# Performance work log

Hardware: AMD Instinct MI355X
Metric: run time of the kernel (lower is better)

Reference implementation:

```python
import jax, jax.numpy as jnp
import numpy as np

B, N, H2, FD, P = 8, 128, 800, 500, 100


def setup_inputs() -> dict:
    key = jax.random.key(0)
    ks = jax.random.split(key, 20)
    w = lambda k, shape, s=0.05: jax.random.normal(k, shape, dtype=jnp.float32) * s
    return {
        "hidden_out": jax.random.normal(ks[0], (B, N, H2), dtype=jnp.float32),
        "Wh": w(ks[1], (FD, H2)), "bh": w(ks[2], (FD,)),
        "Wm": w(ks[3], (FD, H2)), "bm": w(ks[4], (FD,)),
        "Ws": w(ks[5], (FD, H2)), "bs": w(ks[6], (FD,)),
        "Wg": w(ks[7], (FD, H2)), "bg": w(ks[8], (FD,)),
        "W_gp": w(ks[9], (P, 3 * FD)), "b_gp": w(ks[10], (P,)),
        "W_sp": w(ks[11], (P, 3 * FD)), "b_sp": w(ks[12], (P,)),
        "W_rp": w(ks[13], (P, 2 * FD)), "b_rp": w(ks[14], (P,)),
        "w_go": w(ks[15], (1, P)), "b_go": w(ks[16], (1,)),
        "w_so": w(ks[17], (1, P)), "b_so": w(ks[18], (1,)),
    }


def reference(hidden_out, Wh, bh, Wm, bm, Ws, bs, Wg, bg,
              W_gp, b_gp, W_sp, b_sp, W_rp, b_rp,
              w_go, b_go, w_so, b_so):
    # hidden_out: [B, n, 2H]. Scores indexed [b, i(modifier), k(grand/sib), j(head)].
    n = hidden_out.shape[1]
    Fd = Wh.shape[0]
    # tanh(cat(...)) is elementwise, so tanh each per-position projection.
    head = jnp.tanh(jnp.einsum('bnh,fh->bnf', hidden_out, Wh) + bh)
    mod  = jnp.tanh(jnp.einsum('bnh,fh->bnf', hidden_out, Wm) + bm)
    sib  = jnp.tanh(jnp.einsum('bnh,fh->bnf', hidden_out, Ws) + bs)
    grd  = jnp.tanh(jnp.einsum('bnh,fh->bnf', hidden_out, Wg) + bg)

    # grand_out(grand_preout(x)) is a composed linear map (no nonlinearity between),
    # so the score decomposes into per-position scalars.
    vg, vgh, vgm = [(w_go @ W_gp[:, a * Fd:(a + 1) * Fd]).ravel() for a in range(3)]
    c_g = (b_gp @ w_go.ravel()) + b_go[0]
    gk = grd @ vg   # [B, n] grand position k
    gj = head @ vgh  # [B, n] head position j
    gi = mod @ vgm   # [B, n] modifier position i
    grand_val = jnp.tanh(gi[:, :, None, None] + gk[:, None, :, None]
                         + gj[:, None, None, :] + c_g)  # [B, i, k, j]

    vsh, vss, vsm = [(w_so @ W_sp[:, a * Fd:(a + 1) * Fd]).ravel() for a in range(3)]
    c_s = (b_sp @ w_so.ravel()) + b_so[0]
    sk = head @ vsh  # s-head at position k
    sj = sib @ vss   # sibling at position j
    si = mod @ vsm   # s-modifier at position i
    sib_val = jnp.tanh(si[:, :, None, None] + sk[:, None, :, None]
                       + sj[:, None, None, :] + c_s)

    idx = jnp.arange(n)
    i_ = idx[:, None, None]
    k_ = idx[None, :, None]
    j_ = idx[None, None, :]
    valid = (i_ != 0) & (i_ != j_) & (j_ != k_)  # main triple-index branch

    grand_scores = jnp.where(valid, grand_val, -jnp.inf)
    sibling_scores = jnp.where(valid, sib_val, jnp.float32(0.0))

    # root branch: j = k = 0, i != 0; uses root_preout then grand_out.
    r0 = head[:, 0] @ (w_go @ W_rp[:, :Fd]).ravel()        # [B]
    ri = mod @ (w_go @ W_rp[:, Fd:]).ravel()                # [B, n]
    root = jnp.tanh(r0[:, None] + ri + (b_rp @ w_go.ravel()) + b_go[0])
    grand_scores = grand_scores.at[:, 1:, 0, 0].set(root[:, 1:])

    return grand_scores, sibling_scores
```

## Files before the change

### kernel.cpp

```cpp
#include <hip/hip_runtime.h>
#include <math.h>

#define FD 500
#define H2 800
#define NRR 1024
#define NPAD 2048
#define NKS 25

#define NEG_HUGE (-1.0e30f)

typedef __bf16 bf16x8 __attribute__((ext_vector_type(8)));
typedef float f32x4 __attribute__((ext_vector_type(4)));

union ChunkU { uint4 u; bf16x8 b; __bf16 h[8]; };

__device__ __forceinline__ float fast_tanh(float x) {
    float e = __expf(2.0f * x);
    return 1.0f - 2.0f / (e + 1.0f);
}

__device__ __forceinline__ bf16x8 as_frag(uint4 v) { ChunkU c; c.u = v; return c.b; }

__device__ __forceinline__ void gl_lds16(const uint4* g, uint4* lds) {
    __builtin_amdgcn_global_load_lds(
        (const __attribute__((address_space(1))) unsigned int*)g,
        (__attribute__((address_space(3))) unsigned int*)lds,
        16, 0, 0);
}

#define CV_STRIDE 164

__global__ __launch_bounds__(256) void convert_prep_kernel(
        const float* __restrict__ hidden,
        const float* __restrict__ Wh, const float* __restrict__ Wm,
        const float* __restrict__ Ws, const float* __restrict__ Wg,
        uint4* __restrict__ A_t, uint4* __restrict__ B_t,
        const float* __restrict__ W_gp, const float* __restrict__ b_gp,
        const float* __restrict__ W_sp, const float* __restrict__ b_sp,
        const float* __restrict__ W_rp, const float* __restrict__ b_rp,
        const float* __restrict__ w_go, const float* __restrict__ b_go,
        const float* __restrict__ w_so, const float* __restrict__ b_so,
        const float* __restrict__ bh, const float* __restrict__ bm,
        const float* __restrict__ bs, const float* __restrict__ bg,
        float* __restrict__ S8, float* __restrict__ bias_c,
        float* __restrict__ consts) {
    int blk = blockIdx.x;
    int t = threadIdx.x;

    if (blk == 272) {
        __shared__ float cr[3][128];
        if (t < 128) {
            cr[0][t] = (t < 100) ? b_gp[t] * w_go[t] : 0.f;
            cr[1][t] = (t < 100) ? b_sp[t] * w_so[t] : 0.f;
            cr[2][t] = (t < 100) ? b_rp[t] * w_go[t] : 0.f;
        }
        __syncthreads();
        for (int s = 64; s > 0; s >>= 1) {
            if (t < s) {
                cr[0][t] += cr[0][t+s];
                cr[1][t] += cr[1][t+s];
                cr[2][t] += cr[2][t+s];
            }
            __syncthreads();
        }
        if (t == 0) {
            consts[0] = cr[0][0] + b_go[0];
            consts[1] = cr[1][0] + b_so[0];
            consts[2] = cr[2][0] + b_go[0];
        }
        return;
    }

    if (blk >= 240) {
        __shared__ float racc[4][3][64];
        int pb = blk - 240;
        int j = t & 63;
        int e = t >> 6;
        int c = pb*64 + j;

        const float* v0 = nullptr; const float* v1 = nullptr; const float* v2 = nullptr;
        const float* m0 = nullptr; const float* m1 = nullptr; const float* m2 = nullptr;
        int o0 = 0, o1 = 0, o2 = 0, st0 = 0, st1 = 0, st2 = 0;
        int q0 = -1, q1 = -1, q2 = -1;
        float bias = 0.f;
        if (c < 2000) {
            int tt = c / FD, f = c % FD;
            if (tt == 0) {
                q0=1; v0=w_go; m0=W_gp; o0=500+f;  st0=1500;
                q1=5; v1=w_so; m1=W_sp; o1=f;      st1=1500;
                q2=7; v2=w_go; m2=W_rp; o2=f;      st2=1000;
                bias = bh[f];
            } else if (tt == 1) {
                q0=0; v0=w_go; m0=W_gp; o0=1000+f; st0=1500;
                q1=3; v1=w_so; m1=W_sp; o1=1000+f; st1=1500;
                q2=6; v2=w_go; m2=W_rp; o2=500+f;  st2=1000;
                bias = bm[f];
            } else if (tt == 2) {
                q0=4; v0=w_so; m0=W_sp; o0=500+f;  st0=1500;
                bias = bs[f];
            } else {
                q0=2; v0=w_go; m0=W_gp; o0=f;      st0=1500;
                bias = bg[f];
            }
        }
        float s0 = 0.f, s1 = 0.f, s2 = 0.f;
        int p0 = e * 25;
        #pragma unroll 5
        for (int p = p0; p < p0 + 25; ++p) {
            if (v0) s0 += v0[p] * m0[p*st0 + o0];
            if (v1) s1 += v1[p] * m1[p*st1 + o1];
            if (v2) s2 += v2[p] * m2[p*st2 + o2];
        }
        racc[e][0][j] = s0; racc[e][1][j] = s1; racc[e][2][j] = s2;
        __syncthreads();
        if (e == 0) {
            float v[8] = {0,0,0,0,0,0,0,0};
            float r0 = racc[0][0][j] + racc[1][0][j] + racc[2][0][j] + racc[3][0][j];
            float r1 = racc[0][1][j] + racc[1][1][j] + racc[2][1][j] + racc[3][1][j];
            float r2 = racc[0][2][j] + racc[1][2][j] + racc[2][2][j] + racc[3][2][j];
            if (q0 >= 0) v[q0] = r0;
            if (q1 >= 0) v[q1] = r1;
            if (q2 >= 0) v[q2] = r2;
            #pragma unroll
            for (int q = 0; q < 8; ++q) S8[q*NPAD + c] = v[q];
            bias_c[c] = bias;
        }
        return;
    }

    __shared__ float Ls[64 * CV_STRIDE];
    bool isA = blk < 80;
    int tile = isA ? (blk / 5) : ((blk - 80) / 5);
    int slab = isA ? (blk % 5) : ((blk - 80) % 5);

    #pragma unroll
    for (int i = 0; i < 10; ++i) {
        int idx = t + i*256;
        int row = idx / 40;
        int kq  = idx - row*40;
        float4 v = {0.f,0.f,0.f,0.f};
        if (isA) {
            int grow = tile*64 + row;
            v = *(const float4*)(hidden + (size_t)grow*H2 + slab*160 + kq*4);
        } else {
            int c = tile*64 + row;
            if (c < 2000) {
                int wt = c / FD, wf = c % FD;
                const float* wm = (wt==0)?Wh:(wt==1)?Wm:(wt==2)?Ws:Wg;
                v = *(const float4*)(wm + (size_t)wf*H2 + slab*160 + kq*4);
            }
        }
        *(float4*)&Ls[row*CV_STRIDE + kq*4] = v;
    }
    __syncthreads();

    int f = t >> 6, l = t & 63;
    int lrow  = f*16 + (l & 15);
    int koff0 = (l >> 4) * 8;
    uint4* dstbase = (isA ? A_t : B_t) + (size_t)tile * NKS * 512;
    #pragma unroll
    for (int ksl = 0; ksl < 5; ++ksl) {
        int ks = slab*5 + ksl;
        const float* src = &Ls[lrow*CV_STRIDE + ksl*32 + koff0];
        ChunkU hc, lo;
        #pragma unroll
        for (int j = 0; j < 8; ++j) {
            float x = src[j];
            __bf16 h = (__bf16)x;
            hc.h[j] = h;
            lo.h[j] = (__bf16)(x - (float)h);
        }
        uint4* dst = dstbase + (size_t)ks * 512;
        dst[(0*4 + f)*64 + l] = hc.u;
        dst[(1*4 + f)*64 + l] = lo.u;
    }
}

__global__ __launch_bounds__(256, 2) void gemm_kernel(
        const uint4* __restrict__ A_t, const uint4* __restrict__ B_t,
        const float* __restrict__ S8, const float* __restrict__ bias_c,
        float* __restrict__ partials) {
    __shared__ uint4 Abuf[4][512];
    __shared__ uint4 Bbuf[4][512];
    int tid = threadIdx.x;

    int lin = blockIdx.y * 32 + blockIdx.x;
    int xcd = lin & 7;
    int w   = lin >> 3;
    int rb  = (xcd & 1)*8 + (w & 7);
    int cb  = (xcd >> 1)*8 + (w >> 3);

    int l  = tid & 63;
    int wid = tid >> 6;
    int wr = wid >> 1, wc = wid & 1;
    int fa = wr*2, fb = wc*2;

    bool stA = wid < 2;
    int half = wid & 1;
    const uint4* sblk = (stA ? A_t + (size_t)rb * NKS * 512
                             : B_t + (size_t)cb * NKS * 512) + half*256;

    #define STAGE(buf, ks) do { \
        const uint4* sg_ = sblk + (ks)*512 + l; \
        uint4* db_ = (stA ? &Abuf[buf][0] : &Bbuf[buf][0]) + half*256; \
        gl_lds16(sg_,       db_); \
        gl_lds16(sg_ + 64,  db_ + 64); \
        gl_lds16(sg_ + 128, db_ + 128); \
        gl_lds16(sg_ + 192, db_ + 192); } while(0)

    f32x4 acc00 = {0.f,0.f,0.f,0.f}, acc01 = {0.f,0.f,0.f,0.f};
    f32x4 acc10 = {0.f,0.f,0.f,0.f}, acc11 = {0.f,0.f,0.f,0.f};

    #define COMPUTE(cur) do { \
        const uint4* Ab_ = &Abuf[cur][0]; \
        const uint4* Bb_ = &Bbuf[cur][0]; \
        bf16x8 ah0 = as_frag(Ab_[(fa+0)*64+l]), ah1 = as_frag(Ab_[(fa+1)*64+l]); \
        bf16x8 al0 = as_frag(Ab_[(4+fa+0)*64+l]), al1 = as_frag(Ab_[(4+fa+1)*64+l]); \
        bf16x8 bh0 = as_frag(Bb_[(fb+0)*64+l]), bh1 = as_frag(Bb_[(fb+1)*64+l]); \
        bf16x8 bl0 = as_frag(Bb_[(4+fb+0)*64+l]), bl1 = as_frag(Bb_[(4+fb+1)*64+l]); \
        acc00 = __builtin_amdgcn_mfma_f32_16x16x32_bf16(ah0, bh0, acc00,0,0,0); \
        acc00 = __builtin_amdgcn_mfma_f32_16x16x32_bf16(ah0, bl0, acc00,0,0,0); \
        acc00 = __builtin_amdgcn_mfma_f32_16x16x32_bf16(al0, bh0, acc00,0,0,0); \
        acc01 = __builtin_amdgcn_mfma_f32_16x16x32_bf16(ah0, bh1, acc01,0,0,0); \
        acc01 = __builtin_amdgcn_mfma_f32_16x16x32_bf16(ah0, bl1, acc01,0,0,0); \
        acc01 = __builtin_amdgcn_mfma_f32_16x16x32_bf16(al0, bh1, acc01,0,0,0); \
        acc10 = __builtin_amdgcn_mfma_f32_16x16x32_bf16(ah1, bh0, acc10,0,0,0); \
        acc10 = __builtin_amdgcn_mfma_f32_16x16x32_bf16(ah1, bl0, acc10,0,0,0); \
        acc10 = __builtin_amdgcn_mfma_f32_16x16x32_bf16(al1, bh0, acc10,0,0,0); \
        acc11 = __builtin_amdgcn_mfma_f32_16x16x32_bf16(ah1, bh1, acc11,0,0,0); \
        acc11 = __builtin_amdgcn_mfma_f32_16x16x32_bf16(ah1, bl1, acc11,0,0,0); \
        acc11 = __builtin_amdgcn_mfma_f32_16x16x32_bf16(al1, bh1, acc11,0,0,0); } while(0)

    STAGE(0, 0);
    STAGE(1, 1);

    for (int ks = 0; ks < NKS; ++ks) {
        if (ks + 2 < NKS) STAGE((ks + 2) & 3, ks + 2);
        if (ks < NKS - 2) {
            asm volatile("s_waitcnt vmcnt(4)" ::: "memory");
        } else {
            asm volatile("s_waitcnt vmcnt(0)" ::: "memory");
        }
        __builtin_amdgcn_s_barrier();
        __builtin_amdgcn_sched_barrier(0);
        COMPUTE(ks & 3);
    }
    asm volatile("s_waitcnt vmcnt(0) lgkmcnt(0)" ::: "memory");
    __builtin_amdgcn_s_barrier();
    #undef STAGE
    #undef COMPUTE

    int lr = l >> 4, lc = l & 15;
    float* Y = (float*)Abuf;
    {
        int col0 = (wc*2 + 0)*16 + lc;
        int col1 = (wc*2 + 1)*16 + lc;
        float bias0 = bias_c[cb*64 + col0], bias1 = bias_c[cb*64 + col1];
        int rb0 = (wr*2 + 0)*16 + lr*4;
        int rb1 = (wr*2 + 1)*16 + lr*4;
        #pragma unroll
        for (int r=0;r<4;++r) {
            Y[(rb0 + r)*64 + col0] = fast_tanh(acc00[r] + bias0);
            Y[(rb0 + r)*64 + col1] = fast_tanh(acc01[r] + bias1);
            Y[(rb1 + r)*64 + col0] = fast_tanh(acc10[r] + bias0);
            Y[(rb1 + r)*64 + col1] = fast_tanh(acc11[r] + bias1);
        }
    }
    __syncthreads();
    #pragma unroll
    for (int it=0; it<2; ++it) {
        int task = tid + it*256;
        int q = task & 7, row = task >> 3;
        const float4* s8r = (const float4*)(S8 + q*NPAD + cb*64);
        const float4* yr  = (const float4*)(Y + row*64);
        float s = 0.f;
        #pragma unroll
        for (int c4=0;c4<16;++c4) {
            float4 a = yr[c4], b = s8r[c4];
            s += a.x*b.x + a.y*b.y + a.z*b.z + a.w*b.w;
        }
        partials[((size_t)cb*NRR + rb*64 + row)*8 + q] = s;
    }
}

__global__ __launch_bounds__(256) void fill2_kernel(
        const float* __restrict__ partials, const float* __restrict__ consts,
        float* __restrict__ grand, float* __restrict__ sib) {
    int bi = blockIdx.x;
    int b = bi >> 7;
    int i = bi & 127;
    int tid = threadIdx.x;

    __shared__ float ph[256][4];
    __shared__ float gks[128], sks[128], Egj[128], Esj[128];
    __shared__ float own[4];

    {
        int r = tid & 127, half = tid >> 7;
        int grow = b*128 + r;
        float gj=0.f, gk=0.f, sj=0.f, sk=0.f;
        #pragma unroll 4
        for (int cc = 0; cc < 16; ++cc) {
            const float* p = partials + (size_t)(half*16 + cc)*8192 + (size_t)grow*8;
            gj += p[1]; gk += p[2]; sj += p[4]; sk += p[5];
        }
        ph[tid][0]=gj; ph[tid][1]=gk; ph[tid][2]=sj; ph[tid][3]=sk;
    }
    __syncthreads();
    if (tid < 128) {
        float gj = ph[tid][0] + ph[tid+128][0];
        float gk = ph[tid][1] + ph[tid+128][1];
        float sj = ph[tid][2] + ph[tid+128][2];
        float sk = ph[tid][3] + ph[tid+128][3];
        gks[tid] = gk; sks[tid] = sk;
        Egj[tid] = __expf(2.f * gj);
        Esj[tid] = __expf(2.f * sj);
    } else if (tid < 132) {
        int t2 = tid - 128;
        int grow = (t2 == 3) ? b*128 : (b*128 + i);
        int q = (t2==0) ? 0 : (t2==1) ? 3 : (t2==2) ? 6 : 7;
        float s = 0.f;
        #pragma unroll 8
        for (int cbk = 0; cbk < 32; ++cbk)
            s += partials[(size_t)cbk*8192 + (size_t)grow*8 + q];
        own[t2] = s;
    }
    __syncthreads();

    float gic = own[0] + consts[0];
    float sic = own[1] + consts[1];
    float rootv = fast_tanh(own[3] + own[2] + consts[2]);

    size_t base = (size_t)bi * (128*128);
    int j4 = (tid & 31) * 4;
    int klo = tid >> 5;

    for (int it = 0; it < 16; ++it) {
        int k = it*8 + klo;
        float Eg = __expf(2.f * (gic + gks[k]));
        float Es = __expf(2.f * (sic + sks[k]));
        float4 go, so;
        #pragma unroll
        for (int jj = 0; jj < 4; ++jj) {
            int j = j4 + jj;
            bool valid = (i != 0) && (i != j) && (j != k);
            float tg = Eg * Egj[j];
            float ts = Es * Esj[j];
            float g = 1.f - 2.f * __builtin_amdgcn_rcpf(tg + 1.f);
            float s = 1.f - 2.f * __builtin_amdgcn_rcpf(ts + 1.f);
            g = valid ? g : NEG_HUGE;
            s = valid ? s : 0.0f;
            if (i != 0 && k == 0 && j == 0) g = rootv;
            (&go.x)[jj] = g;
            (&so.x)[jj] = s;
        }
        size_t off = base + (size_t)k*128 + j4;
        *(float4*)(grand + off) = go;
        *(float4*)(sib + off) = so;
    }
}

extern "C" void kernel_launch(void* const* d_in, const int* in_sizes, int n_in,
                              void* d_out, int out_size, void* d_ws, size_t ws_size,
                              hipStream_t stream) {
    const float* hidden = (const float*)d_in[0];
    const float* Wh  = (const float*)d_in[1];   const float* bh  = (const float*)d_in[2];
    const float* Wm  = (const float*)d_in[3];   const float* bm  = (const float*)d_in[4];
    const float* Ws_ = (const float*)d_in[5];   const float* bs  = (const float*)d_in[6];
    const float* Wg  = (const float*)d_in[7];   const float* bg  = (const float*)d_in[8];
    const float* W_gp = (const float*)d_in[9];  const float* b_gp = (const float*)d_in[10];
    const float* W_sp = (const float*)d_in[11]; const float* b_sp = (const float*)d_in[12];
    const float* W_rp = (const float*)d_in[13]; const float* b_rp = (const float*)d_in[14];
    const float* w_go = (const float*)d_in[15]; const float* b_go = (const float*)d_in[16];
    const float* w_so = (const float*)d_in[17]; const float* b_so = (const float*)d_in[18];

    float* out   = (float*)d_out;
    float* grand = out;
    float* sib   = out + (size_t)16777216;

    uint4* A_t = (uint4*)out;
    uint4* B_t = (uint4*)out + 204800;

    float* S8      = (float*)d_ws;
    float* bias_c  = S8 + 16384;
    float* consts  = bias_c + 2048;
    float* partials= consts + 16;

    convert_prep_kernel<<<dim3(273), dim3(256), 0, stream>>>(
        hidden, Wh, Wm, Ws_, Wg, A_t, B_t,
        W_gp, b_gp, W_sp, b_sp, W_rp, b_rp, w_go, b_go, w_so, b_so,
        bh, bm, bs, bg, S8, bias_c, consts);
    gemm_kernel<<<dim3(32,16), dim3(256), 0, stream>>>(A_t, B_t, S8, bias_c, partials);
    fill2_kernel<<<dim3(1024), dim3(256), 0, stream>>>(partials, consts, grand, sib);
}
```

Measured before the change: 84.61 us.

## Fuse fp32-to-bf16 hi/lo split into GEMM, loading fp32 directly to LDS

Removes the separate conversion pass that wrote pre-split bf16 hi/lo tiles of hidden and the weights to scratch. The GEMM now streams raw fp32 rows straight into LDS with global_load_lds and splits them into hi/lo bf16 fragments in registers before each MFMA group. This drops one kernel's full read and write of the operands, and the prep kernel shrinks to only the small vector reductions. In exchange the GEMM redoes the conversion once per tile that reuses each operand, and its global loads become strided row reads instead of pre-packed contiguous chunks.

New measurement: 94.26 us. 11.4% more time.

```diff
diff --git a/kernel.cpp b/kernel.cpp
--- a/kernel.cpp
+++ b/kernel.cpp
@@ -19,22 +19,31 @@
     return 1.0f - 2.0f / (e + 1.0f);
 }
 
-__device__ __forceinline__ bf16x8 as_frag(uint4 v) { ChunkU c; c.u = v; return c.b; }
-
-__device__ __forceinline__ void gl_lds16(const uint4* g, uint4* lds) {
+__device__ __forceinline__ void gl_lds16(const float* g, uint4* lds) {
     __builtin_amdgcn_global_load_lds(
         (const __attribute__((address_space(1))) unsigned int*)g,
         (__attribute__((address_space(3))) unsigned int*)lds,
         16, 0, 0);
 }
 
-#define CV_STRIDE 164
-
-__global__ __launch_bounds__(256) void convert_prep_kernel(
-        const float* __restrict__ hidden,
-        const float* __restrict__ Wh, const float* __restrict__ Wm,
-        const float* __restrict__ Ws, const float* __restrict__ Wg,
-        uint4* __restrict__ A_t, uint4* __restrict__ B_t,
+__device__ __forceinline__ void cvt_hilo(uint4 x0, uint4 x1, bf16x8& hi, bf16x8& lo) {
+    union { uint4 u; float f[4]; } a, b;
+    a.u = x0; b.u = x1;
+    ChunkU h, m;
+    #pragma unroll
+    for (int j = 0; j < 4; ++j) {
+        float x = a.f[j]; __bf16 hh = (__bf16)x;
+        h.h[j] = hh; m.h[j] = (__bf16)(x - (float)hh);
+    }
+    #pragma unroll
+    for (int j = 0; j < 4; ++j) {
+        float x = b.f[j]; __bf16 hh = (__bf16)x;
+        h.h[4+j] = hh; m.h[4+j] = (__bf16)(x - (float)hh);
+    }
+    hi = h.b; lo = m.b;
+}
+
+__global__ __launch_bounds__(256) void prep_kernel(
         const float* __restrict__ W_gp, const float* __restrict__ b_gp,
         const float* __restrict__ W_sp, const float* __restrict__ b_sp,
         const float* __restrict__ W_rp, const float* __restrict__ b_rp,
@@ -47,7 +56,7 @@
     int blk = blockIdx.x;
     int t = threadIdx.x;
 
-    if (blk == 272) {
+    if (blk == 32) {
         __shared__ float cr[3][128];
         if (t < 128) {
             cr[0][t] = (t < 100) ? b_gp[t] * w_go[t] : 0.f;
@@ -71,113 +80,64 @@
         return;
     }
 
-    if (blk >= 240) {
-        __shared__ float racc[4][3][64];
-        int pb = blk - 240;
-        int j = t & 63;
-        int e = t >> 6;
-        int c = pb*64 + j;
-
-        const float* v0 = nullptr; const float* v1 = nullptr; const float* v2 = nullptr;
-        const float* m0 = nullptr; const float* m1 = nullptr; const float* m2 = nullptr;
-        int o0 = 0, o1 = 0, o2 = 0, st0 = 0, st1 = 0, st2 = 0;
-        int q0 = -1, q1 = -1, q2 = -1;
-        float bias = 0.f;
-        if (c < 2000) {
-            int tt = c / FD, f = c % FD;
-            if (tt == 0) {
-                q0=1; v0=w_go; m0=W_gp; o0=500+f;  st0=1500;
-                q1=5; v1=w_so; m1=W_sp; o1=f;      st1=1500;
-                q2=7; v2=w_go; m2=W_rp; o2=f;      st2=1000;
-                bias = bh[f];
-            } else if (tt == 1) {
-                q0=0; v0=w_go; m0=W_gp; o0=1000+f; st0=1500;
-                q1=3; v1=w_so; m1=W_sp; o1=1000+f; st1=1500;
-                q2=6; v2=w_go; m2=W_rp; o2=500+f;  st2=1000;
-                bias = bm[f];
-            } else if (tt == 2) {
-                q0=4; v0=w_so; m0=W_sp; o0=500+f;  st0=1500;
-                bias = bs[f];
-            } else {
-                q0=2; v0=w_go; m0=W_gp; o0=f;      st0=1500;
-                bias = bg[f];
-            }
-        }
-        float s0 = 0.f, s1 = 0.f, s2 = 0.f;
-        int p0 = e * 25;
-        #pragma unroll 5
-        for (int p = p0; p < p0 + 25; ++p) {
-            if (v0) s0 += v0[p] * m0[p*st0 + o0];
-            if (v1) s1 += v1[p] * m1[p*st1 + o1];
-            if (v2) s2 += v2[p] * m2[p*st2 + o2];
-        }
-        racc[e][0][j] = s0; racc[e][1][j] = s1; racc[e][2][j] = s2;
-        __syncthreads();
-        if (e == 0) {
-            float v[8] = {0,0,0,0,0,0,0,0};
-            float r0 = racc[0][0][j] + racc[1][0][j] + racc[2][0][j] + racc[3][0][j];
-            float r1 = racc[0][1][j] + racc[1][1][j] + racc[2][1][j] + racc[3][1][j];
-            float r2 = racc[0][2][j] + racc[1][2][j] + racc[2][2][j] + racc[3][2][j];
-            if (q0 >= 0) v[q0] = r0;
-            if (q1 >= 0) v[q1] = r1;
-            if (q2 >= 0) v[q2] = r2;
-            #pragma unroll
-            for (int q = 0; q < 8; ++q) S8[q*NPAD + c] = v[q];
-            bias_c[c] = bias;
-        }
-        return;
-    }
-
-    __shared__ float Ls[64 * CV_STRIDE];
-    bool isA = blk < 80;
-    int tile = isA ? (blk / 5) : ((blk - 80) / 5);
-    int slab = isA ? (blk % 5) : ((blk - 80) % 5);
-
-    #pragma unroll
-    for (int i = 0; i < 10; ++i) {
-        int idx = t + i*256;
-        int row = idx / 40;
-        int kq  = idx - row*40;
-        float4 v = {0.f,0.f,0.f,0.f};
-        if (isA) {
-            int grow = tile*64 + row;
-            v = *(const float4*)(hidden + (size_t)grow*H2 + slab*160 + kq*4);
+    __shared__ float racc[4][3][64];
+    int j = t & 63;
+    int e = t >> 6;
+    int c = blk*64 + j;
+
+    const float* v0 = nullptr; const float* v1 = nullptr; const float* v2 = nullptr;
+    const float* m0 = nullptr; const float* m1 = nullptr; const float* m2 = nullptr;
+    int o0 = 0, o1 = 0, o2 = 0, st0 = 0, st1 = 0, st2 = 0;
+    int q0 = -1, q1 = -1, q2 = -1;
+    float bias = 0.f;
+    if (c < 2000) {
+        int tt = c / FD, f = c % FD;
+        if (tt == 0) {
+            q0=1; v0=w_go; m0=W_gp; o0=500+f;  st0=1500;
+            q1=5; v1=w_so; m1=W_sp; o1=f;      st1=1500;
+            q2=7; v2=w_go; m2=W_rp; o2=f;      st2=1000;
+            bias = bh[f];
+        } else if (tt == 1) {
+            q0=0; v0=w_go; m0=W_gp; o0=1000+f; st0=1500;
+            q1=3; v1=w_so; m1=W_sp; o1=1000+f; st1=1500;
+            q2=6; v2=w_go; m2=W_rp; o2=500+f;  st2=1000;
+            bias = bm[f];
+        } else if (tt == 2) {
+            q0=4; v0=w_so; m0=W_sp; o0=500+f;  st0=1500;
+            bias = bs[f];
         } else {
-            int c = tile*64 + row;
-            if (c < 2000) {
-                int wt = c / FD, wf = c % FD;
-                const float* wm = (wt==0)?Wh:(wt==1)?Wm:(wt==2)?Ws:Wg;
-                v = *(const float4*)(wm + (size_t)wf*H2 + slab*160 + kq*4);
-            }
-        }
-        *(float4*)&Ls[row*CV_STRIDE + kq*4] = v;
-    }
+            q0=2; v0=w_go; m0=W_gp; o0=f;      st0=1500;
+            bias = bg[f];
+        }
+    }
+    float s0 = 0.f, s1 = 0.f, s2 = 0.f;
+    int p0 = e * 25;
+    #pragma unroll 5
+    for (int p = p0; p < p0 + 25; ++p) {
+        if (v0) s0 += v0[p] * m0[p*st0 + o0];
+        if (v1) s1 += v1[p] * m1[p*st1 + o1];
+        if (v2) s2 += v2[p] * m2[p*st2 + o2];
+    }
+    racc[e][0][j] = s0; racc[e][1][j] = s1; racc[e][2][j] = s2;
     __syncthreads();
-
-    int f = t >> 6, l = t & 63;
-    int lrow  = f*16 + (l & 15);
-    int koff0 = (l >> 4) * 8;
-    uint4* dstbase = (isA ? A_t : B_t) + (size_t)tile * NKS * 512;
-    #pragma unroll
-    for (int ksl = 0; ksl < 5; ++ksl) {
-        int ks = slab*5 + ksl;
-        const float* src = &Ls[lrow*CV_STRIDE + ksl*32 + koff0];
-        ChunkU hc, lo;
+    if (e == 0) {
+        float v[8] = {0,0,0,0,0,0,0,0};
+        float r0 = racc[0][0][j] + racc[1][0][j] + racc[2][0][j] + racc[3][0][j];
+        float r1 = racc[0][1][j] + racc[1][1][j] + racc[2][1][j] + racc[3][1][j];
+        float r2 = racc[0][2][j] + racc[1][2][j] + racc[2][2][j] + racc[3][2][j];
+        if (q0 >= 0) v[q0] = r0;
+        if (q1 >= 0) v[q1] = r1;
+        if (q2 >= 0) v[q2] = r2;
         #pragma unroll
-        for (int j = 0; j < 8; ++j) {
-            float x = src[j];
-            __bf16 h = (__bf16)x;
-            hc.h[j] = h;
-            lo.h[j] = (__bf16)(x - (float)h);
-        }
-        uint4* dst = dstbase + (size_t)ks * 512;
-        dst[(0*4 + f)*64 + l] = hc.u;
-        dst[(1*4 + f)*64 + l] = lo.u;
+        for (int q = 0; q < 8; ++q) S8[q*NPAD + c] = v[q];
+        bias_c[c] = bias;
     }
 }
 
 __global__ __launch_bounds__(256, 2) void gemm_kernel(
-        const uint4* __restrict__ A_t, const uint4* __restrict__ B_t,
+        const float* __restrict__ hidden,
+        const float* __restrict__ Wh, const float* __restrict__ Wm,
+        const float* __restrict__ Ws, const float* __restrict__ Wg,
         const float* __restrict__ S8, const float* __restrict__ bias_c,
         float* __restrict__ partials) {
     __shared__ uint4 Abuf[4][512];
@@ -196,17 +156,46 @@
     int fa = wr*2, fb = wc*2;
 
     bool stA = wid < 2;
-    int half = wid & 1;
-    const uint4* sblk = (stA ? A_t + (size_t)rb * NKS * 512
-                             : B_t + (size_t)cb * NKS * 512) + half*256;
+    int fbase = (wid & 1) * 2;
+    int rlo = l & 15;
+    int klane = (l >> 4) * 8;
+
+    const float* src0; const float* src1; const float* src2; const float* src3;
+    {
+        int r0i = (fbase+0)*16 + rlo;
+        int r1i = (fbase+1)*16 + rlo;
+        if (stA) {
+            src0 = hidden + (size_t)(rb*64 + r0i)*H2 + klane;
+            src1 = src0 + 4;
+            src2 = hidden + (size_t)(rb*64 + r1i)*H2 + klane;
+            src3 = src2 + 4;
+        } else {
+            int c0 = cb*64 + r0i, c1 = cb*64 + r1i;
+            if (c0 < 2000) {
+                int wt = c0 / FD, wf = c0 % FD;
+                const float* wm = (wt==0)?Wh:(wt==1)?Wm:(wt==2)?Ws:Wg;
+                src0 = wm + (size_t)wf*H2 + klane;
+            } else src0 = Wh + klane;
+            src1 = src0 + 4;
+            if (c1 < 2000) {
+                int wt = c1 / FD, wf = c1 % FD;
+                const float* wm = (wt==0)?Wh:(wt==1)?Wm:(wt==2)?Ws:Wg;
+                src2 = wm + (size_t)wf*H2 + klane;
+            } else src2 = Wh + klane;
+            src3 = src2 + 4;
+        }
+    }
+    int d0 = ((fbase+0)*2 + 0)*64;
+    int d1 = ((fbase+0)*2 + 1)*64;
+    int d2 = ((fbase+1)*2 + 0)*64;
+    int d3 = ((fbase+1)*2 + 1)*64;
 
     #define STAGE(buf, ks) do { \
-        const uint4* sg_ = sblk + (ks)*512 + l; \
-        uint4* db_ = (stA ? &Abuf[buf][0] : &Bbuf[buf][0]) + half*256; \
-        gl_lds16(sg_,       db_); \
-        gl_lds16(sg_ + 64,  db_ + 64); \
-        gl_lds16(sg_ + 128, db_ + 128); \
-        gl_lds16(sg_ + 192, db_ + 192); } while(0)
+        uint4* db_ = stA ? &Abuf[buf][0] : &Bbuf[buf][0]; \
+        gl_lds16(src0 + (ks)*32, db_ + d0); \
+        gl_lds16(src1 + (ks)*32, db_ + d1); \
+        gl_lds16(src2 + (ks)*32, db_ + d2); \
+        gl_lds16(src3 + (ks)*32, db_ + d3); } while(0)
 
     f32x4 acc00 = {0.f,0.f,0.f,0.f}, acc01 = {0.f,0.f,0.f,0.f};
     f32x4 acc10 = {0.f,0.f,0.f,0.f}, acc11 = {0.f,0.f,0.f,0.f};
@@ -214,10 +203,11 @@
     #define COMPUTE(cur) do { \
         const uint4* Ab_ = &Abuf[cur][0]; \
         const uint4* Bb_ = &Bbuf[cur][0]; \
-        bf16x8 ah0 = as_frag(Ab_[(fa+0)*64+l]), ah1 = as_frag(Ab_[(fa+1)*64+l]); \
-        bf16x8 al0 = as_frag(Ab_[(4+fa+0)*64+l]), al1 = as_frag(Ab_[(4+fa+1)*64+l]); \
-        bf16x8 bh0 = as_frag(Bb_[(fb+0)*64+l]), bh1 = as_frag(Bb_[(fb+1)*64+l]); \
-        bf16x8 bl0 = as_frag(Bb_[(4+fb+0)*64+l]), bl1 = as_frag(Bb_[(4+fb+1)*64+l]); \
+        bf16x8 ah0, al0, ah1, al1, bh0, bl0, bh1, bl1; \
+        cvt_hilo(Ab_[((fa+0)*2+0)*64 + l], Ab_[((fa+0)*2+1)*64 + l], ah0, al0); \
+        cvt_hilo(Ab_[((fa+1)*2+0)*64 + l], Ab_[((fa+1)*2+1)*64 + l], ah1, al1); \
+        cvt_hilo(Bb_[((fb+0)*2+0)*64 + l], Bb_[((fb+0)*2+1)*64 + l], bh0, bl0); \
+        cvt_hilo(Bb_[((fb+1)*2+0)*64 + l], Bb_[((fb+1)*2+1)*64 + l], bh1, bl1); \
         acc00 = __builtin_amdgcn_mfma_f32_16x16x32_bf16(ah0, bh0, acc00,0,0,0); \
         acc00 = __builtin_amdgcn_mfma_f32_16x16x32_bf16(ah0, bl0, acc00,0,0,0); \
         acc00 = __builtin_amdgcn_mfma_f32_16x16x32_bf16(al0, bh0, acc00,0,0,0); \
@@ -378,18 +368,15 @@
     float* grand = out;
     float* sib   = out + (size_t)16777216;
 
-    uint4* A_t = (uint4*)out;
-    uint4* B_t = (uint4*)out + 204800;
-
     float* S8      = (float*)d_ws;
     float* bias_c  = S8 + 16384;
     float* consts  = bias_c + 2048;
     float* partials= consts + 16;
 
-    convert_prep_kernel<<<dim3(273), dim3(256), 0, stream>>>(
-        hidden, Wh, Wm, Ws_, Wg, A_t, B_t,
+    prep_kernel<<<dim3(33), dim3(256), 0, stream>>>(
         W_gp, b_gp, W_sp, b_sp, W_rp, b_rp, w_go, b_go, w_so, b_so,
         bh, bm, bs, bg, S8, bias_c, consts);
-    gemm_kernel<<<dim3(32,16), dim3(256), 0, stream>>>(A_t, B_t, S8, bias_c, partials);
+    gemm_kernel<<<dim3(32,16), dim3(256), 0, stream>>>(
+        hidden, Wh, Wm, Ws_, Wg, S8, bias_c, partials);
     fill2_kernel<<<dim3(1024), dim3(256), 0, stream>>>(partials, consts, grand, sib);
 }
```
